# Kernel tuning notes

Hardware: AMD Instinct MI355X
Metric: run time of the kernel (lower is better)

The kernel has to match this reference:

```python
import jax, jax.numpy as jnp
import numpy as np
from jax import lax

B, T, C, K = 16, 1024, 512, 5
PAD = (K - 1) // 2
EPS_LN = 1e-5
EPS_BN = 1e-5


def setup_inputs() -> dict:
    key = jax.random.key(0)
    ks = jax.random.split(key, 8)
    s1 = 1.0 / np.sqrt(C)          # fan-in of pointwise conv1 (C -> 2C)
    s2 = 1.0 / np.sqrt(2 * C * K)  # fan-in of k=5 conv (2C -> 2C)
    s3 = 1.0 / np.sqrt(C)          # fan-in of pointwise conv3 (C -> C)
    return {
        "x": jax.random.normal(ks[0], (B, T, C), jnp.float32),
        "ln_g": jnp.ones((C,), jnp.float32),
        "ln_b": jnp.zeros((C,), jnp.float32),
        "w1": (jax.random.normal(ks[1], (2 * C, C), jnp.float32) * s1),
        "b1": jnp.zeros((2 * C,), jnp.float32),
        "w2": (jax.random.normal(ks[2], (K, 2 * C, 2 * C), jnp.float32) * s2),  # WIO layout
        "b2": jnp.zeros((2 * C,), jnp.float32),
        "bn_g": jnp.ones((C,), jnp.float32),
        "bn_b": jnp.zeros((C,), jnp.float32),
        "bn_mean": jax.random.normal(ks[3], (C,), jnp.float32) * 0.1,
        "bn_var": jax.random.uniform(ks[4], (C,), jnp.float32, 0.5, 1.5),
        "w3": (jax.random.normal(ks[5], (C, C), jnp.float32) * s3),
        "b3": jnp.zeros((C,), jnp.float32),
    }


def reference(x, ln_g, ln_b, w1, b1, w2, b2, bn_g, bn_b, bn_mean, bn_var, w3, b3):
    # LayerNorm over channel dim (B, T, C)
    mu = jnp.mean(x, axis=-1, keepdims=True)
    var = jnp.mean(jnp.square(x - mu), axis=-1, keepdims=True)
    h = (x - mu) * lax.rsqrt(var + EPS_LN) * ln_g + ln_b

    # pointwise conv C -> 2C (kernel 1 == GEMM), then Swish
    h = jnp.einsum('btc,oc->bto', h, w1) + b1        # (B, T, 2C)
    h = h * jax.nn.sigmoid(h)

    # kernel-5 conv 2C -> 2C, 'same' padding, channels-last
    h = lax.conv_general_dilated(
        h, w2, window_strides=(1,), padding=[(PAD, PAD)],
        dimension_numbers=('NWC', 'WIO', 'NWC')) + b2  # (B, T, 2C)

    # GLU over channel dim: first half * sigmoid(second half)
    a, g = h[..., :C], h[..., C:]
    h = a * jax.nn.sigmoid(g)                        # (B, T, C)

    # BatchNorm1d(C), eval mode (running stats)
    h = (h - bn_mean) * lax.rsqrt(bn_var + EPS_BN) * bn_g + bn_b

    # pointwise conv C -> C; dropout is identity at inference.
    # Torch output is sequential(...)(B,C,T).transpose(1,2) -> (B, T, C)
    return jnp.einsum('btc,oc->bto', h, w3) + b3
```

## Files before the change

### kernel.cpp

```cpp
#include <hip/hip_runtime.h>
#include <cstdint>


#define NB    16
#define TT    1024
#define CC    512
#define C2    1024
#define TPAD  1028

typedef unsigned short u16;
typedef short bf16x8 __attribute__((ext_vector_type(8)));
typedef float f32x4  __attribute__((ext_vector_type(4)));

__device__ __forceinline__ float bf2f(u16 u) {
  union { unsigned int i; float f; } v; v.i = ((unsigned int)u) << 16; return v.f;
}
__device__ __forceinline__ u16 f2bf(float f) {
  union { float f; unsigned int i; } v; v.f = f;
  unsigned int x = v.i;
  return (u16)((x + 0x7fffu + ((x >> 16) & 1u)) >> 16);
}

__global__ __launch_bounds__(256) void prep_k(
    const float* __restrict__ w1, u16* __restrict__ w1b,
    const float* __restrict__ w3, u16* __restrict__ w3b,
    u16* __restrict__ h1p) {
  const int b = blockIdx.x;
  if (b < 512) {
    const int i = (b * 256 + threadIdx.x) * 4;
    float4 v = *(const float4*)(w1 + i);
    u16 o[4] = { f2bf(v.x), f2bf(v.y), f2bf(v.z), f2bf(v.w) };
    *(uint2*)(w1b + i) = *(const uint2*)o;
  } else if (b < 768) {
    const int i = ((b - 512) * 256 + threadIdx.x) * 4;
    float4 v = *(const float4*)(w3 + i);
    u16 o[4] = { f2bf(v.x), f2bf(v.y), f2bf(v.z), f2bf(v.w) };
    *(uint2*)(w3b + i) = *(const uint2*)o;
  } else {
    const int idx = (b - 768) * 256 + threadIdx.x;
    const int bb  = idx >> 9;
    const int rem = idx & 511;
    const int ri  = rem >> 7;
    const int c8  = (rem & 127) * 8;
    const int row = bb * TPAD + (ri < 2 ? ri : 1024 + ri);
    uint4 z = make_uint4(0u, 0u, 0u, 0u);
    *(uint4*)(h1p + (size_t)row * C2 + c8) = z;
  }
}

__global__ void transpose_w2(const float* __restrict__ w2, u16* __restrict__ w2t) {
  __shared__ u16 t[64][65];
  const int k  = blockIdx.z;
  const int i0 = blockIdx.x * 64, o0 = blockIdx.y * 64;
  const int tx = threadIdx.x, ty = threadIdx.y;
  for (int r = ty; r < 64; r += 4)
    t[r][tx] = f2bf(w2[((size_t)(k * C2) + i0 + r) * C2 + o0 + tx]);
  __syncthreads();
  for (int r = ty; r < 64; r += 4)
    w2t[((size_t)(k * C2) + o0 + r) * C2 + i0 + tx] = t[tx][r];
}

__global__ __launch_bounds__(256) void layernorm_k(
    const float* __restrict__ x, const float* __restrict__ lng,
    const float* __restrict__ lnb, u16* __restrict__ out) {
  const int tok  = blockIdx.x * 4 + (threadIdx.x >> 6);
  const int lane = threadIdx.x & 63;
  const float* xp = x + (size_t)tok * CC + lane * 8;
  float f[8];
  *(float4*)(f)     = *(const float4*)(xp);
  *(float4*)(f + 4) = *(const float4*)(xp + 4);
  float s = 0.f, s2 = 0.f;
#pragma unroll
  for (int j = 0; j < 8; j++) { s += f[j]; s2 += f[j] * f[j]; }
#pragma unroll
  for (int m = 32; m >= 1; m >>= 1) { s += __shfl_xor(s, m, 64); s2 += __shfl_xor(s2, m, 64); }
  const float mu  = s  * (1.f / 512.f);
  const float var = s2 * (1.f / 512.f) - mu * mu;
  const float rs  = rsqrtf(var + 1e-5f);
  u16 ov[8];
#pragma unroll
  for (int j = 0; j < 8; j++) {
    const int c = lane * 8 + j;
    ov[j] = f2bf((f[j] - mu) * rs * lng[c] + lnb[c]);
  }
  *(uint4*)(out + (size_t)tok * CC + lane * 8) = *(const uint4*)ov;
}

template <int EPI>
__global__ __launch_bounds__(256, 3) void gemm_bt(
    const u16* __restrict__ A, const u16* __restrict__ Bt,
    const float* __restrict__ bias, void* __restrict__ outv,
    const int Kd, const int ldA) {
  __shared__ __align__(16) u16 smem[20480];
  const int tid  = threadIdx.x;
  const int m0   = blockIdx.x * 128;
  const int n0   = blockIdx.y * 128;
  const int wave = tid >> 6, lane = tid & 63;
  const int wm = (wave & 1) * 64, wn = (wave >> 1) * 64;
  const int quad = lane >> 4, l16 = lane & 15;
  const int row = tid >> 2;
  const int kc  = (tid & 3) * 8;
  const int J = Kd >> 5;

  const u16* Ap0 = A + (size_t)(m0 + row) * ldA + kc;
  const u16* Ap1 = Ap0 + (size_t)64 * ldA;
  const u16* Bp0 = Bt + (size_t)(n0 + row) * Kd + kc;
  const u16* Bp1 = Bp0 + (size_t)64 * Kd;

  f32x4 acc[4][4] = {};
  uint4 rA0 = *(const uint4*)Ap0, rA1 = *(const uint4*)Ap1;
  uint4 rB0 = *(const uint4*)Bp0, rB1 = *(const uint4*)Bp1;
  *(uint4*)(smem + row * 40 + kc)                = rA0;
  *(uint4*)(smem + (64 + row) * 40 + kc)         = rA1;
  *(uint4*)(smem + 10240 + row * 40 + kc)        = rB0;
  *(uint4*)(smem + 10240 + (64 + row) * 40 + kc) = rB1;
  rA0 = *(const uint4*)(Ap0 + 32); rA1 = *(const uint4*)(Ap1 + 32);
  rB0 = *(const uint4*)(Bp0 + 32); rB1 = *(const uint4*)(Bp1 + 32);
  __syncthreads();

#pragma unroll 1
  for (int j = 0; j < J; j++) {
    const u16* curA = smem + (j & 1) * 5120;
    const u16* curB = smem + 10240 + (j & 1) * 5120;
    if (j + 1 < J) {
      u16* nxtA = smem + ((j + 1) & 1) * 5120;
      u16* nxtB = smem + 10240 + ((j + 1) & 1) * 5120;
      *(uint4*)(nxtA + row * 40 + kc)        = rA0;
      *(uint4*)(nxtA + (64 + row) * 40 + kc) = rA1;
      *(uint4*)(nxtB + row * 40 + kc)        = rB0;
      *(uint4*)(nxtB + (64 + row) * 40 + kc) = rB1;
    }
    {
      const int k2 = (j + 2 < J) ? (j + 2) * 32 : 0;
      rA0 = *(const uint4*)(Ap0 + k2); rA1 = *(const uint4*)(Ap1 + k2);
      rB0 = *(const uint4*)(Bp0 + k2); rB1 = *(const uint4*)(Bp1 + k2);
    }
    bf16x8 af[4], bfr[4];
#pragma unroll
    for (int i = 0; i < 4; i++)
      af[i] = *(const bf16x8*)(curA + (wm + i * 16 + l16) * 40 + quad * 8);
#pragma unroll
    for (int i = 0; i < 4; i++)
      bfr[i] = *(const bf16x8*)(curB + (wn + i * 16 + l16) * 40 + quad * 8);
#pragma unroll
    for (int mi = 0; mi < 4; mi++)
#pragma unroll
      for (int ni = 0; ni < 4; ni++)
        acc[mi][ni] = __builtin_amdgcn_mfma_f32_16x16x32_bf16(
            af[mi], bfr[ni], acc[mi][ni], 0, 0, 0);
    __syncthreads();
  }

  float bv[4];
#pragma unroll
  for (int ni = 0; ni < 4; ni++) bv[ni] = bias[n0 + wn + ni * 16 + l16];

  if (EPI == 0) {
    u16* epi = smem + wave * 4608;
#pragma unroll
    for (int mi = 0; mi < 4; mi++)
#pragma unroll
      for (int ni = 0; ni < 4; ni++)
#pragma unroll
        for (int r = 0; r < 4; r++) {
          float v = acc[mi][ni][r] + bv[ni];
          v = v / (1.f + __expf(-v));
          epi[(mi * 16 + quad * 4 + r) * 72 + ni * 16 + l16] = f2bf(v);
        }
    u16* h1p = (u16*)outv;
#pragma unroll
    for (int p = 0; p < 8; p++) {
      const int rrow = p * 8 + (lane >> 3);
      const int colb = (lane & 7) * 8;
      uint4 v = *(const uint4*)(epi + rrow * 72 + colb);
      const int rr = m0 + wm + rrow;
      const int bb = rr >> 10, tt = rr & 1023;
      *(uint4*)(h1p + (size_t)(bb * TPAD + tt + 2) * C2 + n0 + wn + colb) = v;
    }
  } else {
    float* fepi = (float*)(smem + wave * 4608);
    float* outf = (float*)outv;
#pragma unroll
    for (int mi = 0; mi < 4; mi++) {
      float* fp = fepi + (mi & 1) * 1088;
#pragma unroll
      for (int ni = 0; ni < 4; ni++)
#pragma unroll
        for (int r = 0; r < 4; r++)
          fp[(quad * 4 + r) * 68 + ni * 16 + l16] = acc[mi][ni][r] + bv[ni];
#pragma unroll
      for (int p = 0; p < 4; p++) {
        const int rrow = p * 4 + (lane >> 4);
        const int col  = (lane & 15) * 4;
        float4 v = *(const float4*)(fp + rrow * 68 + col);
        *(float4*)(outf + (size_t)(m0 + wm + mi * 16 + rrow) * CC + n0 + wn + col) = v;
      }
    }
  }
}

__global__ __launch_bounds__(256, 2) void conv5_mfma(
    const u16* __restrict__ h1p, const u16* __restrict__ w2t,
    const float* __restrict__ b2, u16* __restrict__ out) {
  __shared__ __align__(16) u16 smem[31040];
  const int tid = threadIdx.x;
  const int mt  = blockIdx.x;
  const int n0  = blockIdx.y * 128;
  const int bb  = mt >> 3;
  const int t0  = (mt & 7) * 128;
  const size_t arow0 = (size_t)bb * TPAD + t0;
  const int wave = tid >> 6, lane = tid & 63;
  const int wm = (wave & 1) * 64, wn = (wave >> 1) * 64;
  const int quad = lane >> 4, l16 = lane & 15;
  const int row = tid >> 2;
  const int kc  = (tid & 3) * 8;
  u16* lsB = smem + 10560;

  const u16* Ap0 = h1p + (arow0 + row) * C2 + kc;
  const u16* Ap1 = Ap0 + (size_t)64 * C2;
  const u16* Ap2 = h1p + (arow0 + 128 + row) * C2 + kc;

  f32x4 acc[4][4] = {};
  uint4 rA0, rA1, rA2, rB0, rB1, rB2, rB3, rB4, rB5, rB6, rB7, rB8, rB9;

#define BGLD(R, Q, I0) { const int u = ((Q) & 1) * 256 + tid;                  \
    R = *(const uint4*)(w2t + (size_t)(((Q) >> 1) * C2 + n0 + (u >> 2)) * C2   \
                        + (I0) + (u & 3) * 8); }
#define BSTF(R, Q) { const int u = ((Q) & 1) * 256 + tid; const int nn = u >> 2; \
    *(uint4*)(lsB + ((Q) >> 1) * 4096 + (nn >> 4) * 512                        \
              + ((u & 3) * 16 + (nn & 15)) * 8) = R; }
#define BGLD_ALL(I0) BGLD(rB0,0,I0) BGLD(rB1,1,I0) BGLD(rB2,2,I0) \
    BGLD(rB3,3,I0) BGLD(rB4,4,I0) BGLD(rB5,5,I0) BGLD(rB6,6,I0)   \
    BGLD(rB7,7,I0) BGLD(rB8,8,I0) BGLD(rB9,9,I0)
#define BSTF_ALL() BSTF(rB0,0) BSTF(rB1,1) BSTF(rB2,2) BSTF(rB3,3) \
    BSTF(rB4,4) BSTF(rB5,5) BSTF(rB6,6) BSTF(rB7,7) BSTF(rB8,8) BSTF(rB9,9)

  rA0 = *(const uint4*)Ap0; rA1 = *(const uint4*)Ap1;
  if (tid < 16) rA2 = *(const uint4*)Ap2;
  *(uint4*)(smem + row * 40 + kc)        = rA0;
  *(uint4*)(smem + (64 + row) * 40 + kc) = rA1;
  if (tid < 16) *(uint4*)(smem + (128 + row) * 40 + kc) = rA2;
  BGLD_ALL(0)
  rA0 = *(const uint4*)(Ap0 + 32); rA1 = *(const uint4*)(Ap1 + 32);
  if (tid < 16) rA2 = *(const uint4*)(Ap2 + 32);

#pragma unroll 1
  for (int j = 0; j < 32; j++) {
    __syncthreads();
    BSTF_ALL()
    {
      u16* nxtA = smem + ((j + 1) & 1) * 5280;
      *(uint4*)(nxtA + row * 40 + kc)        = rA0;
      *(uint4*)(nxtA + (64 + row) * 40 + kc) = rA1;
      if (tid < 16) *(uint4*)(nxtA + (128 + row) * 40 + kc) = rA2;
    }
    __syncthreads();
    {
      const int ib = (j + 1 < 32) ? (j + 1) * 32 : 0;
      BGLD_ALL(ib)
      const int ia = (j + 2 < 32) ? (j + 2) * 32 : 0;
      rA0 = *(const uint4*)(Ap0 + ia);
      rA1 = *(const uint4*)(Ap1 + ia);
      if (tid < 16) rA2 = *(const uint4*)(Ap2 + ia);
    }
    const u16* curA = smem + (j & 1) * 5280;
#pragma unroll
    for (int k = 0; k < 5; k++) {
      bf16x8 af[4], bfr[4];
#pragma unroll
      for (int i = 0; i < 4; i++)
        af[i] = *(const bf16x8*)(curA + (wm + i * 16 + l16 + k) * 40 + quad * 8);
#pragma unroll
      for (int i = 0; i < 4; i++)
        bfr[i] = *(const bf16x8*)(lsB + k * 4096 + ((wn >> 4) + i) * 512 + lane * 8);
#pragma unroll
      for (int mi = 0; mi < 4; mi++)
#pragma unroll
        for (int ni = 0; ni < 4; ni++)
          acc[mi][ni] = __builtin_amdgcn_mfma_f32_16x16x32_bf16(
              af[mi], bfr[ni], acc[mi][ni], 0, 0, 0);
    }
  }
#undef BGLD
#undef BSTF
#undef BGLD_ALL
#undef BSTF_ALL
  __syncthreads();

  float bv[4];
#pragma unroll
  for (int ni = 0; ni < 4; ni++) bv[ni] = b2[n0 + wn + ni * 16 + l16];

  u16* epi = smem + wave * 4608;
#pragma unroll
  for (int mi = 0; mi < 4; mi++)
#pragma unroll
    for (int ni = 0; ni < 4; ni++)
#pragma unroll
      for (int r = 0; r < 4; r++)
        epi[(mi * 16 + quad * 4 + r) * 72 + ni * 16 + l16] = f2bf(acc[mi][ni][r] + bv[ni]);

  const size_t orow0 = (size_t)bb * TT + t0;
#pragma unroll
  for (int p = 0; p < 8; p++) {
    const int rrow = p * 8 + (lane >> 3);
    const int colb = (lane & 7) * 8;
    uint4 v = *(const uint4*)(epi + rrow * 72 + colb);
    *(uint4*)(out + (orow0 + wm + rrow) * C2 + n0 + wn + colb) = v;
  }
}

__global__ __launch_bounds__(256) void glu_bn_k(
    const u16* __restrict__ hc, const float* __restrict__ bg,
    const float* __restrict__ bb_, const float* __restrict__ bm,
    const float* __restrict__ bv, u16* __restrict__ out) {
  const int idx = blockIdx.x * 256 + threadIdx.x;
  const int r  = idx >> 6;
  const int c8 = (idx & 63) * 8;
  const u16* pa = hc + (size_t)r * C2 + c8;
  uint4 ra = *(const uint4*)pa;
  uint4 rg = *(const uint4*)(pa + CC);
  u16 av[8], gv[8], ov[8];
  *(uint4*)av = ra; *(uint4*)gv = rg;
#pragma unroll
  for (int j = 0; j < 8; j++) {
    const int c = c8 + j;
    const float a = bf2f(av[j]);
    const float g = bf2f(gv[j]);
    const float h = a / (1.f + __expf(-g));
    const float sc = bg[c] * rsqrtf(bv[c] + 1e-5f);
    ov[j] = f2bf((h - bm[c]) * sc + bb_[c]);
  }
  *(uint4*)(out + (size_t)r * CC + c8) = *(const uint4*)ov;
}

extern "C" void kernel_launch(void* const* d_in, const int* in_sizes, int n_in,
                              void* d_out, int out_size, void* d_ws, size_t ws_size,
                              hipStream_t stream) {
  const float* x   = (const float*)d_in[0];
  const float* lng = (const float*)d_in[1];
  const float* lnb = (const float*)d_in[2];
  const float* w1  = (const float*)d_in[3];
  const float* b1  = (const float*)d_in[4];
  const float* w2  = (const float*)d_in[5];
  const float* b2  = (const float*)d_in[6];
  const float* bng = (const float*)d_in[7];
  const float* bnb = (const float*)d_in[8];
  const float* bnm = (const float*)d_in[9];
  const float* bnv = (const float*)d_in[10];
  const float* w3  = (const float*)d_in[11];
  const float* b3  = (const float*)d_in[12];

  u16* ws  = (u16*)d_ws;
  u16* hln = ws;
  u16* h2  = hln;
  u16* h1p = ws + 8388608;
  u16* w2t = h1p + 16842752;
  u16* hcv = w2t + 5242880;
  u16* w1b = hcv + 16777216;
  u16* w3b = w1b + 524288;

  prep_k      <<<800, 256, 0, stream>>>(w1, w1b, w3, w3b, h1p);
  transpose_w2<<<dim3(16, 16, 5), dim3(64, 4), 0, stream>>>(w2, w2t);
  layernorm_k <<<4096, 256, 0, stream>>>(x, lng, lnb, hln);
  gemm_bt<0>  <<<dim3(128, 8), 256, 0, stream>>>(hln, w1b, b1, h1p, 512, 512);
  conv5_mfma  <<<dim3(128, 8), 256, 0, stream>>>(h1p, w2t, b2, hcv);
  glu_bn_k    <<<4096, 256, 0, stream>>>(hcv, bng, bnb, bnm, bnv, h2);
  gemm_bt<1>  <<<dim3(128, 4), 256, 0, stream>>>(h2, w3b, b3, d_out, 512, 512);
}
```

Before: 360.9 us.

## Fuse GLU and BatchNorm into conv5 epilogue with direct-to-LDS weight loads

The k=5 conv kernel now computes paired 'a' and 'gate' channel tiles in each block (64 columns from each half), so GLU and eval-mode BatchNorm run in the epilogue. This removes the separate glu_bn kernel and the round trip of the full 2C-wide bf16 conv output through global memory. The tile grows to 256x128 with one block per CU, and weight tiles are staged with global_load_lds DMA into double-buffered LDS. The larger LDS footprint and lower occupancy may reduce latency hiding.

```diff
diff --git a/kernel.cpp b/kernel.cpp
--- a/kernel.cpp
+++ b/kernel.cpp
@@ -19,6 +19,11 @@
   union { float f; unsigned int i; } v; v.f = f;
   unsigned int x = v.i;
   return (u16)((x + 0x7fffu + ((x >> 16) & 1u)) >> 16);
+}
+__device__ __forceinline__ void gload16(const u16* g, u16* l) {
+  __builtin_amdgcn_global_load_lds(
+      (const __attribute__((address_space(1))) unsigned int*)g,
+      (__attribute__((address_space(3))) unsigned int*)l, 16, 0, 0);
 }
 
 __global__ __launch_bounds__(256) void prep_k(
@@ -199,139 +204,140 @@
   }
 }
 
-__global__ __launch_bounds__(256, 2) void conv5_mfma(
+__global__ __launch_bounds__(256, 1) void conv5_fused(
     const u16* __restrict__ h1p, const u16* __restrict__ w2t,
-    const float* __restrict__ b2, u16* __restrict__ out) {
-  __shared__ __align__(16) u16 smem[31040];
+    const float* __restrict__ b2, const float* __restrict__ bng,
+    const float* __restrict__ bnb, const float* __restrict__ bnm,
+    const float* __restrict__ bnv, u16* __restrict__ h2) {
+  __shared__ __align__(16) u16 smem[61760];
   const int tid = threadIdx.x;
   const int mt  = blockIdx.x;
-  const int n0  = blockIdx.y * 128;
-  const int bb  = mt >> 3;
-  const int t0  = (mt & 7) * 128;
+  const int n0  = blockIdx.y * 64;
+  const int bb  = mt >> 2;
+  const int t0  = (mt & 3) * 256;
   const size_t arow0 = (size_t)bb * TPAD + t0;
   const int wave = tid >> 6, lane = tid & 63;
-  const int wm = (wave & 1) * 64, wn = (wave >> 1) * 64;
+  const int wm = (wave & 1) * 128;
+  const int wn = (wave >> 1) * 64;
   const int quad = lane >> 4, l16 = lane & 15;
   const int row = tid >> 2;
   const int kc  = (tid & 3) * 8;
-  u16* lsB = smem + 10560;
+  u16* lsB = smem + 20800;
 
   const u16* Ap0 = h1p + (arow0 + row) * C2 + kc;
   const u16* Ap1 = Ap0 + (size_t)64 * C2;
-  const u16* Ap2 = h1p + (arow0 + 128 + row) * C2 + kc;
-
-  f32x4 acc[4][4] = {};
-  uint4 rA0, rA1, rA2, rB0, rB1, rB2, rB3, rB4, rB5, rB6, rB7, rB8, rB9;
-
-#define BGLD(R, Q, I0) { const int u = ((Q) & 1) * 256 + tid;                  \
-    R = *(const uint4*)(w2t + (size_t)(((Q) >> 1) * C2 + n0 + (u >> 2)) * C2   \
-                        + (I0) + (u & 3) * 8); }
-#define BSTF(R, Q) { const int u = ((Q) & 1) * 256 + tid; const int nn = u >> 2; \
-    *(uint4*)(lsB + ((Q) >> 1) * 4096 + (nn >> 4) * 512                        \
-              + ((u & 3) * 16 + (nn & 15)) * 8) = R; }
-#define BGLD_ALL(I0) BGLD(rB0,0,I0) BGLD(rB1,1,I0) BGLD(rB2,2,I0) \
-    BGLD(rB3,3,I0) BGLD(rB4,4,I0) BGLD(rB5,5,I0) BGLD(rB6,6,I0)   \
-    BGLD(rB7,7,I0) BGLD(rB8,8,I0) BGLD(rB9,9,I0)
-#define BSTF_ALL() BSTF(rB0,0) BSTF(rB1,1) BSTF(rB2,2) BSTF(rB3,3) \
-    BSTF(rB4,4) BSTF(rB5,5) BSTF(rB6,6) BSTF(rB7,7) BSTF(rB8,8) BSTF(rB9,9)
-
-  rA0 = *(const uint4*)Ap0; rA1 = *(const uint4*)Ap1;
-  if (tid < 16) rA2 = *(const uint4*)Ap2;
-  *(uint4*)(smem + row * 40 + kc)        = rA0;
-  *(uint4*)(smem + (64 + row) * 40 + kc) = rA1;
-  if (tid < 16) *(uint4*)(smem + (128 + row) * 40 + kc) = rA2;
-  BGLD_ALL(0)
-  rA0 = *(const uint4*)(Ap0 + 32); rA1 = *(const uint4*)(Ap1 + 32);
-  if (tid < 16) rA2 = *(const uint4*)(Ap2 + 32);
+  const u16* Ap2 = Ap0 + (size_t)128 * C2;
+  const u16* Ap3 = Ap0 + (size_t)192 * C2;
+  const u16* Ap4 = h1p + (arow0 + 256 + (tid >> 2)) * C2 + (tid & 3) * 8;
+
+  const size_t laneterm = (size_t)l16 * 1024 + (size_t)quad * 8;
+
+#define BDMA(Q, I0, DST) {                                                    \
+    const int f_ = wave * 10 + (Q);                                           \
+    const int tap_ = f_ >> 3, nb_ = f_ & 7;                                   \
+    const size_t uni_ = ((size_t)tap_ * 1024 +                                \
+        (size_t)(n0 + nb_ * 16 + ((nb_ >= 4) ? 448 : 0))) * 1024 + (I0);      \
+    gload16(w2t + uni_ + laneterm, (DST) + f_ * 512); }
+#define BDMA_ALL(I0, DST) BDMA(0,I0,DST) BDMA(1,I0,DST) BDMA(2,I0,DST) \
+    BDMA(3,I0,DST) BDMA(4,I0,DST) BDMA(5,I0,DST) BDMA(6,I0,DST)        \
+    BDMA(7,I0,DST) BDMA(8,I0,DST) BDMA(9,I0,DST)
+#define ASTORE(DST) {                                                         \
+    *(uint4*)((DST) + row * 40 + kc)         = rA0;                           \
+    *(uint4*)((DST) + (64 + row) * 40 + kc)  = rA1;                           \
+    *(uint4*)((DST) + (128 + row) * 40 + kc) = rA2;                           \
+    *(uint4*)((DST) + (192 + row) * 40 + kc) = rA3;                           \
+    if (tid < 16)                                                             \
+      *(uint4*)((DST) + (256 + (tid >> 2)) * 40 + (tid & 3) * 8) = rA4; }
+#define ALOAD(I0) {                                                           \
+    rA0 = *(const uint4*)(Ap0 + (I0)); rA1 = *(const uint4*)(Ap1 + (I0));     \
+    rA2 = *(const uint4*)(Ap2 + (I0)); rA3 = *(const uint4*)(Ap3 + (I0));     \
+    if (tid < 16) rA4 = *(const uint4*)(Ap4 + (I0)); }
+
+  f32x4 acc[8][4] = {};
+  uint4 rA0, rA1, rA2, rA3, rA4;
+
+  ALOAD(0)
+  ASTORE(smem)
+  BDMA_ALL(0, lsB)
+  ALOAD(32)
+  __syncthreads();
 
 #pragma unroll 1
   for (int j = 0; j < 32; j++) {
-    __syncthreads();
-    BSTF_ALL()
-    {
-      u16* nxtA = smem + ((j + 1) & 1) * 5280;
-      *(uint4*)(nxtA + row * 40 + kc)        = rA0;
-      *(uint4*)(nxtA + (64 + row) * 40 + kc) = rA1;
-      if (tid < 16) *(uint4*)(nxtA + (128 + row) * 40 + kc) = rA2;
-    }
-    __syncthreads();
-    {
-      const int ib = (j + 1 < 32) ? (j + 1) * 32 : 0;
-      BGLD_ALL(ib)
+    if (j + 1 < 32) {
+      BDMA_ALL((j + 1) * 32, lsB + ((j + 1) & 1) * 20480)
+      ASTORE(smem + ((j + 1) & 1) * 10400)
       const int ia = (j + 2 < 32) ? (j + 2) * 32 : 0;
-      rA0 = *(const uint4*)(Ap0 + ia);
-      rA1 = *(const uint4*)(Ap1 + ia);
-      if (tid < 16) rA2 = *(const uint4*)(Ap2 + ia);
-    }
-    const u16* curA = smem + (j & 1) * 5280;
+      ALOAD(ia)
+    }
+    const u16* curA = smem + (j & 1) * 10400;
+    const u16* curB = lsB + (j & 1) * 20480;
 #pragma unroll
     for (int k = 0; k < 5; k++) {
-      bf16x8 af[4], bfr[4];
+      bf16x8 af[8], bfr[4];
+#pragma unroll
+      for (int i = 0; i < 8; i++)
+        af[i] = *(const bf16x8*)(curA + (wm + i * 16 + l16 + k) * 40 + quad * 8);
 #pragma unroll
       for (int i = 0; i < 4; i++)
-        af[i] = *(const bf16x8*)(curA + (wm + i * 16 + l16 + k) * 40 + quad * 8);
-#pragma unroll
-      for (int i = 0; i < 4; i++)
-        bfr[i] = *(const bf16x8*)(lsB + k * 4096 + ((wn >> 4) + i) * 512 + lane * 8);
-#pragma unroll
-      for (int mi = 0; mi < 4; mi++)
+        bfr[i] = *(const bf16x8*)(curB + (k * 8 + (wn >> 4) + i) * 512 + lane * 8);
+#pragma unroll
+      for (int mi = 0; mi < 8; mi++)
 #pragma unroll
         for (int ni = 0; ni < 4; ni++)
           acc[mi][ni] = __builtin_amdgcn_mfma_f32_16x16x32_bf16(
               af[mi], bfr[ni], acc[mi][ni], 0, 0, 0);
     }
-  }
-#undef BGLD
-#undef BSTF
-#undef BGLD_ALL
-#undef BSTF_ALL
+    __syncthreads();
+  }
+#undef BDMA
+#undef BDMA_ALL
+#undef ASTORE
+#undef ALOAD
+
+  float bv[4];
+#pragma unroll
+  for (int ni = 0; ni < 4; ni++) {
+    const int c = wn + ni * 16 + l16;
+    bv[ni] = b2[n0 + c + ((c >= 64) ? 448 : 0)];
+  }
+  u16* epi = smem;
+#pragma unroll
+  for (int mi = 0; mi < 8; mi++)
+#pragma unroll
+    for (int ni = 0; ni < 4; ni++)
+#pragma unroll
+      for (int r = 0; r < 4; r++)
+        epi[(wm + mi * 16 + quad * 4 + r) * 136 + wn + ni * 16 + l16] =
+            f2bf(acc[mi][ni][r] + bv[ni]);
   __syncthreads();
 
-  float bv[4];
-#pragma unroll
-  for (int ni = 0; ni < 4; ni++) bv[ni] = b2[n0 + wn + ni * 16 + l16];
-
-  u16* epi = smem + wave * 4608;
-#pragma unroll
-  for (int mi = 0; mi < 4; mi++)
-#pragma unroll
-    for (int ni = 0; ni < 4; ni++)
-#pragma unroll
-      for (int r = 0; r < 4; r++)
-        epi[(mi * 16 + quad * 4 + r) * 72 + ni * 16 + l16] = f2bf(acc[mi][ni][r] + bv[ni]);
-
+  const int col8 = (tid & 7) * 8;
+  const int r0   = tid >> 3;
+  float sc[8], off[8];
+#pragma unroll
+  for (int c = 0; c < 8; c++) {
+    const int gc = n0 + col8 + c;
+    const float s = bng[gc] * rsqrtf(bnv[gc] + 1e-5f);
+    sc[c] = s; off[c] = bnb[gc] - bnm[gc] * s;
+  }
   const size_t orow0 = (size_t)bb * TT + t0;
 #pragma unroll
-  for (int p = 0; p < 8; p++) {
-    const int rrow = p * 8 + (lane >> 3);
-    const int colb = (lane & 7) * 8;
-    uint4 v = *(const uint4*)(epi + rrow * 72 + colb);
-    *(uint4*)(out + (orow0 + wm + rrow) * C2 + n0 + wn + colb) = v;
-  }
-}
-
-__global__ __launch_bounds__(256) void glu_bn_k(
-    const u16* __restrict__ hc, const float* __restrict__ bg,
-    const float* __restrict__ bb_, const float* __restrict__ bm,
-    const float* __restrict__ bv, u16* __restrict__ out) {
-  const int idx = blockIdx.x * 256 + threadIdx.x;
-  const int r  = idx >> 6;
-  const int c8 = (idx & 63) * 8;
-  const u16* pa = hc + (size_t)r * C2 + c8;
-  uint4 ra = *(const uint4*)pa;
-  uint4 rg = *(const uint4*)(pa + CC);
-  u16 av[8], gv[8], ov[8];
-  *(uint4*)av = ra; *(uint4*)gv = rg;
-#pragma unroll
-  for (int j = 0; j < 8; j++) {
-    const int c = c8 + j;
-    const float a = bf2f(av[j]);
-    const float g = bf2f(gv[j]);
-    const float h = a / (1.f + __expf(-g));
-    const float sc = bg[c] * rsqrtf(bv[c] + 1e-5f);
-    ov[j] = f2bf((h - bm[c]) * sc + bb_[c]);
-  }
-  *(uint4*)(out + (size_t)r * CC + c8) = *(const uint4*)ov;
+  for (int ro = 0; ro < 8; ro++) {
+    const int r = r0 + ro * 32;
+    uint4 ua = *(const uint4*)(epi + r * 136 + col8);
+    uint4 ug = *(const uint4*)(epi + r * 136 + 64 + col8);
+    u16 av[8], gv[8], ov[8];
+    *(uint4*)av = ua; *(uint4*)gv = ug;
+#pragma unroll
+    for (int c = 0; c < 8; c++) {
+      const float a = bf2f(av[c]);
+      const float g = bf2f(gv[c]);
+      const float h = a / (1.f + __expf(-g));
+      ov[c] = f2bf(h * sc[c] + off[c]);
+    }
+    *(uint4*)(h2 + (orow0 + r) * CC + n0 + col8) = *(const uint4*)ov;
+  }
 }
 
 extern "C" void kernel_launch(void* const* d_in, const int* in_sizes, int n_in,
@@ -356,15 +362,13 @@
   u16* h2  = hln;
   u16* h1p = ws + 8388608;
   u16* w2t = h1p + 16842752;
-  u16* hcv = w2t + 5242880;
-  u16* w1b = hcv + 16777216;
+  u16* w1b = w2t + 5242880;
   u16* w3b = w1b + 524288;
 
   prep_k      <<<800, 256, 0, stream>>>(w1, w1b, w3, w3b, h1p);
   transpose_w2<<<dim3(16, 16, 5), dim3(64, 4), 0, stream>>>(w2, w2t);
   layernorm_k <<<4096, 256, 0, stream>>>(x, lng, lnb, hln);
   gemm_bt<0>  <<<dim3(128, 8), 256, 0, stream>>>(hln, w1b, b1, h1p, 512, 512);
-  conv5_mfma  <<<dim3(128, 8), 256, 0, stream>>>(h1p, w2t, b2, hcv);
-  glu_bn_k    <<<4096, 256, 0, stream>>>(hcv, bng, bnb, bnm, bnv, h2);
+  conv5_fused <<<dim3(64, 8), 256, 0, stream>>>(h1p, w2t, b2, bng, bnb, bnm, bnv, h2);
   gemm_bt<1>  <<<dim3(128, 4), 256, 0, stream>>>(h2, w3b, b3, d_out, 512, 512);
 }
```

Result: no change. 363.9 us (+0.8%).
